# Kernel optimization log

Measured on AMD Instinct MI355X. Metric: run time of the kernel, lower is better.

## Reference

```python
import jax, jax.numpy as jnp
import numpy as np

N_NODES = 100000
N_EDGES = 3200000
D = 32


def _gat(x, edge_index, W, att_s, att_d, bias, heads, ch, neg_slope):
    """PyG-style GATConv (shared lin for src/dst, add_self_loops=False).
    x: [N, D_in], edge_index: [2, E], W: [heads*ch, D_in],
    att_s/att_d: [heads, ch], bias: [heads*ch]. Returns [N, heads*ch]."""
    n = x.shape[0]
    h = (x @ W.T).reshape(n, heads, ch)                      # [N,H,C]
    a_s = (h * att_s[None]).sum(-1)                           # [N,H]
    a_d = (h * att_d[None]).sum(-1)                           # [N,H]
    src, dst = edge_index[0], edge_index[1]
    logits = jax.nn.leaky_relu(a_s[src] + a_d[dst], neg_slope)  # [E,H]
    # segment softmax over edges grouped by destination node
    m = jax.ops.segment_max(logits, dst, num_segments=n)     # [N,H]
    m = jnp.where(jnp.isfinite(m), m, 0.0)                    # nodes w/ no in-edges
    ex = jnp.exp(logits - m[dst])                             # [E,H]
    denom = jax.ops.segment_sum(ex, dst, num_segments=n)     # [N,H]
    alpha = ex / (denom[dst] + 1e-16)                         # [E,H]
    out = jax.ops.segment_sum(alpha[:, :, None] * h[src], dst, num_segments=n)  # [N,H,C]
    return out.reshape(n, heads * ch) + bias


def setup_inputs() -> dict:
    key = jax.random.key(0)
    ks = jax.random.split(key, 16)
    x = jax.random.normal(ks[0], (N_NODES, D), dtype=jnp.float32)
    edge_index = jax.random.randint(ks[1], (2, N_EDGES), 0, N_NODES, dtype=jnp.int64)
    s = 1.0 / np.sqrt(D)
    return {
        "x": x,
        "edge_index": edge_index,
        "W1": jax.random.normal(ks[2], (32, D), dtype=jnp.float32) * s,
        "att_s1": jax.random.normal(ks[3], (2, 16), dtype=jnp.float32) * 0.05,
        "att_d1": jax.random.normal(ks[4], (2, 16), dtype=jnp.float32) * 0.05,
        "b1": jnp.full((32,), 0.1, dtype=jnp.float32),
        "ea1": jnp.ones((1,), dtype=jnp.float32),  # edge_activator
        "W2": jax.random.normal(ks[5], (32, 32), dtype=jnp.float32) * s,
        "att_s2": jax.random.normal(ks[6], (2, 16), dtype=jnp.float32) * 0.05,
        "att_d2": jax.random.normal(ks[7], (2, 16), dtype=jnp.float32) * 0.05,
        "b2": jnp.full((32,), 0.1, dtype=jnp.float32),
        "W3": jax.random.normal(ks[8], (32, 32), dtype=jnp.float32) * s,
        "att_s3": jax.random.normal(ks[9], (1, 32), dtype=jnp.float32) * 0.05,
        "att_d3": jax.random.normal(ks[10], (1, 32), dtype=jnp.float32) * 0.05,
        "b3": jnp.full((32,), 0.1, dtype=jnp.float32),
    }


def reference(x, edge_index, W1, att_s1, att_d1, b1, ea1,
              W2, att_s2, att_d2, b2, W3, att_s3, att_d3, b3):
    # --- layer 1 (negative_slope=0.01) ---
    h = _gat(x, edge_index, W1, att_s1, att_d1, b1, heads=2, ch=16, neg_slope=0.01)
    scale = jnp.tanh(ea1)[0]
    scale = jnp.where(scale < 0.1, 1.0, scale)  # 'continue' branch skips the scaling
    h = h * scale
    h = h + 0.05 * jax.lax.stop_gradient(h)      # h + 0.05*h.detach()
    h = jax.nn.elu(h)                            # eval path (training=False)
    h = jnp.clip(h, -3.0, 3.0)
    # --- layer 2 (default negative_slope=0.2) ---
    h = _gat(h, edge_index, W2, att_s2, att_d2, b2, heads=2, ch=16, neg_slope=0.2)
    h = jax.nn.elu(h)
    h = jnp.clip(h, -3.0, 3.0)
    # --- layer 3: heads=1, concat=False ---
    out = _gat(h, edge_index, W3, att_s3, att_d3, b3, heads=1, ch=32, neg_slope=0.2)
    return out
```

## Files before the change

kernel.cpp:

```cpp
#include <hip/hip_runtime.h>
#include <hip/hip_bf16.h>
#include <hip/hip_fp16.h>


#define NPB  128
#define CAPB 6144
#define PAD_SENTINEL 0xFFFFFFFFu

__global__ void __launch_bounds__(1024)
k_bin(const int* __restrict__ src, const int* __restrict__ dst,
      int* __restrict__ bucket_cursor, unsigned int* __restrict__ pairs,
      int e, int nb) {
    __shared__ int h[1024];
    __shared__ int bs[1024];
    __shared__ int cb[1024];
    __shared__ unsigned int stage[8192];
    int t = threadIdx.x;
    h[t] = 0;
    __syncthreads();
    int e4 = e >> 2;
    int base4 = blockIdx.x * 2048;
    int boff[8];
    unsigned int pk[8];
#pragma unroll
    for (int k = 0; k < 2; k++) {
        int i4 = base4 + k * 1024 + t;
        if (i4 < e4) {
            int4 dv = ((const int4*)dst)[i4];
            int4 sv = ((const int4*)src)[i4];
            const int* dd = (const int*)&dv;
            const int* ss = (const int*)&sv;
#pragma unroll
            for (int j = 0; j < 4; j++) {
                int q = 4 * k + j;
                int d = dd[j];
                int b = d >> 7;
                pk[q] = ((unsigned int)ss[j] << 7) | (unsigned int)(d & 127);
                int off = atomicAdd(&h[b], 1);
                boff[q] = (b << 16) | off;
            }
        } else {
#pragma unroll
            for (int j = 0; j < 4; j++) boff[4 * k + j] = -1;
        }
    }
    __syncthreads();
    if (t >= 128 && t - 128 < nb) {
        int b = t - 128;
        int c = h[b];
        cb[b] = c ? atomicAdd(&bucket_cursor[b], c) : 0;
    }
    if (t < 64) {
        int sum = 0;
#pragma unroll
        for (int j = 0; j < 16; j++) sum += h[t * 16 + j];
        int run = sum;
#pragma unroll
        for (int off = 1; off < 64; off <<= 1) {
            int v = __shfl_up(run, off, 64);
            if (t >= off) run += v;
        }
        int base = run - sum;
#pragma unroll
        for (int j = 0; j < 16; j++) {
            int b = t * 16 + j;
            bs[b] = base;
            base += h[b];
        }
    }
    __syncthreads();
#pragma unroll
    for (int q = 0; q < 8; q++) {
        if (boff[q] >= 0) {
            int b = boff[q] >> 16;
            stage[bs[b] + (boff[q] & 0xFFFF)] = pk[q];
        }
    }
    __syncthreads();
    int wv = t >> 6, ln = t & 63;
    for (int b = wv; b < nb; b += 16) {
        int c = h[b];
        if (c == 0) continue;
        int gb = cb[b];
        int room = CAPB - gb;
        if (c > room) c = (room > 0) ? room : 0;
        unsigned int* dp = pairs + (size_t)b * CAPB + gb;
        const unsigned int* sp = stage + bs[b];
        for (int o = ln; o < c; o += 64) dp[o] = sp[o];
    }
    if (blockIdx.x == 0 && t < (e & 3)) {
        int i = (e & ~3) + t;
        int d = dst[i];
        int b = d >> 7;
        int r = atomicAdd(&bucket_cursor[b], 1);
        if (r < CAPB)
            pairs[(size_t)b * CAPB + r] =
                ((unsigned int)src[i] << 7) | (unsigned int)(d & 127);
    }
}

__global__ void __launch_bounds__(512)
k_bucket_sort(const unsigned int* __restrict__ pairs,
              const int* __restrict__ bucket_cursor,
              int2* __restrict__ rowinfo, int* __restrict__ src_sorted,
              int n) {
    __shared__ int cnt[NPB];
    __shared__ int cur[NPB];
    __shared__ int total;
    __shared__ unsigned int lp[CAPB];
    __shared__ int op[CAPB];
    int b = blockIdx.x;
    int t = threadIdx.x;
    int bbase = b * CAPB;
    int m = bucket_cursor[b];
    if (m > CAPB) m = CAPB;
    if (t < NPB) cnt[t] = 0;
    __syncthreads();
    for (int cb = 0; cb < m; cb += 4096) {
        unsigned int pv[8];
#pragma unroll
        for (int u = 0; u < 8; u++) {
            int i = cb + u * 512 + t;
            pv[u] = (i < m) ? pairs[bbase + i] : PAD_SENTINEL;
        }
#pragma unroll
        for (int u = 0; u < 8; u++) {
            int i = cb + u * 512 + t;
            if (i < m) lp[i] = pv[u];
            if (pv[u] != PAD_SENTINEL) atomicAdd(&cnt[pv[u] & 127], 1);
        }
    }
    __syncthreads();
    if (t < 64) {
        int c0 = cnt[2 * t];
        int c1 = cnt[2 * t + 1];
        int sum = c0 + c1;
        int run = sum;
#pragma unroll
        for (int off = 1; off < 64; off <<= 1) {
            int v = __shfl_up(run, off, 64);
            if (t >= off) run += v;
        }
        int ex = run - sum;
        cur[2 * t] = ex;
        cur[2 * t + 1] = ex + c0;
        int node = b * NPB + 2 * t;
        if (node < n) rowinfo[node] = make_int2(bbase + ex, c0);
        if (node + 1 < n) rowinfo[node + 1] = make_int2(bbase + ex + c0, c1);
        if (t == 63) total = run;
    }
    __syncthreads();
    for (int cb = 0; cb < m; cb += 4096) {
        unsigned int pv[8];
        int of[8];
#pragma unroll
        for (int u = 0; u < 8; u++) {
            int i = cb + u * 512 + t;
            pv[u] = (i < m) ? lp[i] : PAD_SENTINEL;
        }
#pragma unroll
        for (int u = 0; u < 8; u++)
            if (pv[u] != PAD_SENTINEL) of[u] = atomicAdd(&cur[pv[u] & 127], 1);
#pragma unroll
        for (int u = 0; u < 8; u++)
            if (pv[u] != PAD_SENTINEL) op[of[u]] = (int)(pv[u] >> 7);
    }
    __syncthreads();
    int nt4 = (total + 3) >> 2;
    int4* dst4 = (int4*)(src_sorted + bbase);
    const int4* src4 = (const int4*)op;
    for (int i = t; i < nt4; i += 512) dst4[i] = src4[i];
}

template <int H>
__global__ void k_transform(const float* __restrict__ in, const float* __restrict__ W,
                            const float* __restrict__ att_s, const float* __restrict__ att_d,
                            __half* __restrict__ h16, float* __restrict__ a_s,
                            float* __restrict__ a_d, int n) {
    constexpr int C = 32 / H;
    __shared__ float Wl[32][33];
    __shared__ float xs[8][32];
    int t = threadIdx.x;
    for (int i = t; i < 1024; i += 256) Wl[i >> 5][i & 31] = W[i];
    int nl = t >> 5, o = t & 31;
    int node = blockIdx.x * 8 + nl;
    xs[nl][o] = (node < n) ? in[node * 32 + o] : 0.f;
    __syncthreads();
    float acc = 0.f;
#pragma unroll
    for (int k = 0; k < 32; k++) acc = fmaf(xs[nl][k], Wl[o][k], acc);
    if (node < n) {
        h16[node * 32 + o] = __float2half_rn(acc);
        float vs = acc * att_s[o];
        float vd = acc * att_d[o];
#pragma unroll
        for (int m = C / 2; m >= 1; m >>= 1) {
            vs += __shfl_xor(vs, m, 64);
            vd += __shfl_xor(vd, m, 64);
        }
        if ((o % C) == 0) {
            int hh = o / C;
            a_s[node * H + hh] = vs;
            a_d[node * H + hh] = vd;
        }
    }
}

template <int H, int EPI>
__global__ void k_edge(const int2* __restrict__ rowinfo, const int* __restrict__ src_sorted,
                       const __half* __restrict__ h16,
                       const float* __restrict__ a_s, const float* __restrict__ a_d,
                       const float* __restrict__ bias, const float* __restrict__ ea,
                       float* __restrict__ out, int n, float slope) {
    constexpr int CAP = 128;
    constexpr int RSTR = 2 * CAP + 16;
    __shared__ int lds_raw[8][H][RSTR];
    int nw = threadIdx.x >> 5;
    int hl = threadIdx.x & 31;
    int node = blockIdx.x * 8 + nw;
    if (node >= n) return;
    int2 bi = rowinfo[node];
    int beg = bi.x, deg = bi.y;
    int padB = (deg + 31) & ~31;

    float ad[H];
#pragma unroll
    for (int hh = 0; hh < H; hh++) ad[hh] = a_d[node * H + hh];

    float ds[H];
#pragma unroll
    for (int hh = 0; hh < H; hh++) ds[hh] = 0.f;
    bool fast = (padB <= CAP);
    if (fast) {
        for (int idx = hl; idx < padB; idx += 32) {
            if (idx < deg) {
                int s = src_sorted[beg + idx];
                if (H == 2) {
                    float2 as2 = *(const float2*)((const char*)a_s + (unsigned)(s << 3));
                    float l0 = as2.x + ad[0]; l0 = fmaxf(l0, l0 * slope);
                    float l1 = as2.y + ad[1]; l1 = fmaxf(l1, l1 * slope);
                    float e0 = __expf(l0), e1 = __expf(l1);
                    ds[0] += e0; ds[1] += e1;
                    ((int2*)lds_raw[nw][0])[idx] = make_int2(s, __float_as_int(e0));
                    ((int2*)lds_raw[nw][H - 1])[idx] = make_int2(s, __float_as_int(e1));
                } else {
                    float l0 = a_s[s] + ad[0]; l0 = fmaxf(l0, l0 * slope);
                    float e0 = __expf(l0);
                    ds[0] += e0;
                    ((int2*)lds_raw[nw][0])[idx] = make_int2(s, __float_as_int(e0));
                }
            } else {
#pragma unroll
                for (int hh = 0; hh < H; hh++)
                    ((int2*)lds_raw[nw][hh])[idx] = make_int2(0, 0);
            }
        }
    } else {
        for (int idx = hl; idx < deg; idx += 32) {
            int s = src_sorted[beg + idx];
            if (H == 2) {
                float2 as2 = *(const float2*)((const char*)a_s + (unsigned)(s << 3));
                float l0 = as2.x + ad[0]; l0 = fmaxf(l0, l0 * slope);
                float l1 = as2.y + ad[1]; l1 = fmaxf(l1, l1 * slope);
                ds[0] += __expf(l0); ds[1] += __expf(l1);
            } else {
                float l0 = a_s[s] + ad[0]; l0 = fmaxf(l0, l0 * slope);
                ds[0] += __expf(l0);
            }
        }
    }

    int e2 = hl >> 4;
    int l16 = hl & 15;
    int hd = (H == 2) ? (l16 >> 3) : 0;
    int co = l16 << 2;
    float adh = ad[hd];
    float acc0 = 0.f, acc1 = 0.f;
    const char* hbase = (const char*)h16;
    const int* lb = &lds_raw[nw][hd][e2 * 4];

    if (fast) {
        for (int base = 0; base < padB; base += 32) {
            int4 q[8];
#pragma unroll
            for (int u = 0; u < 8; u++)
                q[u] = *(const int4*)(lb + base * 2 + u * 8);
            __half2 hv[16];
#pragma unroll
            for (int u = 0; u < 8; u++) {
                hv[2 * u]     = *(const __half2*)(hbase + (unsigned)((q[u].x << 6) + co));
                hv[2 * u + 1] = *(const __half2*)(hbase + (unsigned)((q[u].z << 6) + co));
            }
#pragma unroll
            for (int u = 0; u < 8; u++) {
                float x0 = __int_as_float(q[u].y);
                float x1 = __int_as_float(q[u].w);
                acc0 = fmaf(x0, __half2float(__low2half(hv[2 * u])), acc0);
                acc1 = fmaf(x0, __half2float(__high2half(hv[2 * u])), acc1);
                acc0 = fmaf(x1, __half2float(__low2half(hv[2 * u + 1])), acc0);
                acc1 = fmaf(x1, __half2float(__high2half(hv[2 * u + 1])), acc1);
            }
        }
    } else {
        for (int base = 0; base < deg; base += 16) {
#pragma unroll
            for (int u = 0; u < 8; u++) {
                int idx = base + u * 2 + e2;
                int s = 0;
                float ex = 0.f;
                if (idx < deg) {
                    s = src_sorted[beg + idx];
                    float l = a_s[s * H + hd] + adh;
                    l = fmaxf(l, l * slope);
                    ex = __expf(l);
                }
                __half2 hv = *(const __half2*)(hbase + (unsigned)((s << 6) + co));
                acc0 = fmaf(ex, __half2float(__low2half(hv)), acc0);
                acc1 = fmaf(ex, __half2float(__high2half(hv)), acc1);
            }
        }
    }

#pragma unroll
    for (int hh = 0; hh < H; hh++) {
        float v = ds[hh];
#pragma unroll
        for (int m = 16; m >= 1; m >>= 1) v += __shfl_xor(v, m, 64);
        ds[hh] = 1.f / (v + 1e-16f);
    }

    acc0 += __shfl_xor(acc0, 16, 64);
    acc1 += __shfl_xor(acc1, 16, 64);

    if (l16 == hl) {
        float invd = ds[hd];
        float2 bv = *(const float2*)(bias + l16 * 2);
        float v0 = fmaf(acc0, invd, bv.x);
        float v1 = fmaf(acc1, invd, bv.y);
        if (EPI == 1) {
            float s0 = tanhf(ea[0]);
            if (s0 < 0.1f) s0 = 1.0f;
            s0 *= 1.05f;
            v0 *= s0; v1 *= s0;
            v0 = (v0 > 0.f) ? v0 : expm1f(v0);
            v1 = (v1 > 0.f) ? v1 : expm1f(v1);
            v0 = fminf(3.f, fmaxf(-3.f, v0));
            v1 = fminf(3.f, fmaxf(-3.f, v1));
        } else if (EPI == 2) {
            v0 = (v0 > 0.f) ? v0 : expm1f(v0);
            v1 = (v1 > 0.f) ? v1 : expm1f(v1);
            v0 = fminf(3.f, fmaxf(-3.f, v0));
            v1 = fminf(3.f, fmaxf(-3.f, v1));
        }
        *(float2*)(out + (size_t)node * 32 + l16 * 2) = make_float2(v0, v1);
    }
}

extern "C" void kernel_launch(void* const* d_in, const int* in_sizes, int n_in,
                              void* d_out, int out_size, void* d_ws, size_t ws_size,
                              hipStream_t stream) {
    const float* x   = (const float*)d_in[0];
    const int*   ei  = (const int*)d_in[1];
    const float* W1  = (const float*)d_in[2];
    const float* as1 = (const float*)d_in[3];
    const float* ad1 = (const float*)d_in[4];
    const float* b1  = (const float*)d_in[5];
    const float* ea1 = (const float*)d_in[6];
    const float* W2  = (const float*)d_in[7];
    const float* as2 = (const float*)d_in[8];
    const float* ad2 = (const float*)d_in[9];
    const float* b2  = (const float*)d_in[10];
    const float* W3  = (const float*)d_in[11];
    const float* as3 = (const float*)d_in[12];
    const float* ad3 = (const float*)d_in[13];
    const float* b3  = (const float*)d_in[14];
    float* out = (float*)d_out;

    const int n = in_sizes[0] / 32;
    const int e = in_sizes[1] / 2;
    const int* src = ei;
    const int* dst = ei + e;
    const int nb = (n + NPB - 1) / NPB;

    char* w = (char*)d_ws;
    auto alloc = [&](size_t bytes) -> void* {
        void* p = (void*)w;
        w += (bytes + 255) & ~(size_t)255;
        return p;
    };
    __half* h16     = (__half*)alloc((size_t)n * 32 * 2);
    float* a_s      = (float*)alloc((size_t)n * 2 * 4);
    float* a_d      = (float*)alloc((size_t)n * 2 * 4);
    float* bufA     = (float*)alloc((size_t)n * 32 * 4);
    float* bufB     = (float*)alloc((size_t)n * 32 * 4);
    int2* rowinfo   = (int2*)alloc((size_t)n * 8);
    int* bucket_cur = (int*)alloc((size_t)(nb + 1) * 4);
    int* src_sorted = (int*)alloc((size_t)nb * CAPB * 4);
    unsigned int* pairs = (unsigned int*)bufA;

    hipMemsetAsync(bucket_cur, 0, (size_t)nb * 4, stream);
    int e4 = e >> 2;
    k_bin<<<(e4 + 2047) / 2048, 1024, 0, stream>>>(src, dst, bucket_cur, pairs, e, nb);
    k_bucket_sort<<<nb, 512, 0, stream>>>(pairs, bucket_cur, rowinfo, src_sorted, n);

    const int tgrid = (n + 7) / 8;
    const int egrid = (n + 7) / 8;

    k_transform<2><<<tgrid, 256, 0, stream>>>(x, W1, as1, ad1, h16, a_s, a_d, n);
    k_edge<2, 1><<<egrid, 256, 0, stream>>>(rowinfo, src_sorted, h16, a_s, a_d, b1, ea1, bufA, n, 0.01f);

    k_transform<2><<<tgrid, 256, 0, stream>>>(bufA, W2, as2, ad2, h16, a_s, a_d, n);
    k_edge<2, 2><<<egrid, 256, 0, stream>>>(rowinfo, src_sorted, h16, a_s, a_d, b2, nullptr, bufB, n, 0.2f);

    k_transform<1><<<tgrid, 256, 0, stream>>>(bufB, W3, as3, ad3, h16, a_s, a_d, n);
    k_edge<1, 0><<<egrid, 256, 0, stream>>>(rowinfo, src_sorted, h16, a_s, a_d, b3, nullptr, out, n, 0.2f);
}
```

Baseline: 346.1 us.

## Split fp16 features into per-half planes and process each half in separate blocks

The transformed fp16 features are stored as two planes of 16 channels each, and a_s/a_d become head-major. The edge-kernel grid is doubled so each block aggregates one channel half (or one head) for 8 nodes. This halves the gather working set per pass so it is more likely to stay in L2, and each warp now covers 4 edges per step with 8 lanes per row. In exchange, the edge indices are read and the logits and exps are computed twice per edge. Nontemporal loads for src_sorted and nontemporal output stores are also added.

```diff
diff --git a/kernel.cpp b/kernel.cpp
--- a/kernel.cpp
+++ b/kernel.cpp
@@ -175,8 +175,8 @@
 template <int H>
 __global__ void k_transform(const float* __restrict__ in, const float* __restrict__ W,
                             const float* __restrict__ att_s, const float* __restrict__ att_d,
-                            __half* __restrict__ h16, float* __restrict__ a_s,
-                            float* __restrict__ a_d, int n) {
+                            __half* __restrict__ h16a, __half* __restrict__ h16b,
+                            float* __restrict__ a_s, float* __restrict__ a_d, int n) {
     constexpr int C = 32 / H;
     __shared__ float Wl[32][33];
     __shared__ float xs[8][32];
@@ -190,7 +190,8 @@
 #pragma unroll
     for (int k = 0; k < 32; k++) acc = fmaf(xs[nl][k], Wl[o][k], acc);
     if (node < n) {
-        h16[node * 32 + o] = __float2half_rn(acc);
+        __half* hp = (o < 16) ? h16a : h16b;
+        hp[node * 16 + (o & 15)] = __float2half_rn(acc);
         float vs = acc * att_s[o];
         float vd = acc * att_d[o];
 #pragma unroll
@@ -200,121 +201,99 @@
         }
         if ((o % C) == 0) {
             int hh = o / C;
-            a_s[node * H + hh] = vs;
-            a_d[node * H + hh] = vd;
+            a_s[hh * n + node] = vs;
+            a_d[hh * n + node] = vd;
         }
     }
 }
 
 template <int H, int EPI>
 __global__ void k_edge(const int2* __restrict__ rowinfo, const int* __restrict__ src_sorted,
-                       const __half* __restrict__ h16,
+                       const __half* __restrict__ h16a, const __half* __restrict__ h16b,
                        const float* __restrict__ a_s, const float* __restrict__ a_d,
                        const float* __restrict__ bias, const float* __restrict__ ea,
                        float* __restrict__ out, int n, float slope) {
     constexpr int CAP = 128;
     constexpr int RSTR = 2 * CAP + 16;
-    __shared__ int lds_raw[8][H][RSTR];
+    __shared__ int lds_raw[8][RSTR];
+    int head = blockIdx.x & 1;
+    int grp = blockIdx.x >> 1;
     int nw = threadIdx.x >> 5;
     int hl = threadIdx.x & 31;
-    int node = blockIdx.x * 8 + nw;
+    int node = grp * 8 + nw;
     if (node >= n) return;
     int2 bi = rowinfo[node];
     int beg = bi.x, deg = bi.y;
-    int padB = (deg + 31) & ~31;
-
-    float ad[H];
-#pragma unroll
-    for (int hh = 0; hh < H; hh++) ad[hh] = a_d[node * H + hh];
-
-    float ds[H];
-#pragma unroll
-    for (int hh = 0; hh < H; hh++) ds[hh] = 0.f;
+    int padB = (deg + 15) & ~15;
+
+    const __half* hsrc = head ? h16b : h16a;
+    const float* asp = a_s + (H == 2 ? head * n : 0);
+    float adv = a_d[(H == 2 ? head * n : 0) + node];
+
+    float dsum = 0.f;
     bool fast = (padB <= CAP);
     if (fast) {
         for (int idx = hl; idx < padB; idx += 32) {
             if (idx < deg) {
-                int s = src_sorted[beg + idx];
-                if (H == 2) {
-                    float2 as2 = *(const float2*)((const char*)a_s + (unsigned)(s << 3));
-                    float l0 = as2.x + ad[0]; l0 = fmaxf(l0, l0 * slope);
-                    float l1 = as2.y + ad[1]; l1 = fmaxf(l1, l1 * slope);
-                    float e0 = __expf(l0), e1 = __expf(l1);
-                    ds[0] += e0; ds[1] += e1;
-                    ((int2*)lds_raw[nw][0])[idx] = make_int2(s, __float_as_int(e0));
-                    ((int2*)lds_raw[nw][H - 1])[idx] = make_int2(s, __float_as_int(e1));
-                } else {
-                    float l0 = a_s[s] + ad[0]; l0 = fmaxf(l0, l0 * slope);
-                    float e0 = __expf(l0);
-                    ds[0] += e0;
-                    ((int2*)lds_raw[nw][0])[idx] = make_int2(s, __float_as_int(e0));
-                }
+                int s = __builtin_nontemporal_load(src_sorted + beg + idx);
+                float l = asp[s] + adv;
+                l = fmaxf(l, l * slope);
+                float e0 = __expf(l);
+                dsum += e0;
+                ((int2*)lds_raw[nw])[idx] = make_int2(s, __float_as_int(e0));
             } else {
-#pragma unroll
-                for (int hh = 0; hh < H; hh++)
-                    ((int2*)lds_raw[nw][hh])[idx] = make_int2(0, 0);
+                ((int2*)lds_raw[nw])[idx] = make_int2(0, 0);
             }
         }
     } else {
         for (int idx = hl; idx < deg; idx += 32) {
-            int s = src_sorted[beg + idx];
-            if (H == 2) {
-                float2 as2 = *(const float2*)((const char*)a_s + (unsigned)(s << 3));
-                float l0 = as2.x + ad[0]; l0 = fmaxf(l0, l0 * slope);
-                float l1 = as2.y + ad[1]; l1 = fmaxf(l1, l1 * slope);
-                ds[0] += __expf(l0); ds[1] += __expf(l1);
-            } else {
-                float l0 = a_s[s] + ad[0]; l0 = fmaxf(l0, l0 * slope);
-                ds[0] += __expf(l0);
-            }
-        }
-    }
-
-    int e2 = hl >> 4;
-    int l16 = hl & 15;
-    int hd = (H == 2) ? (l16 >> 3) : 0;
-    int co = l16 << 2;
-    float adh = ad[hd];
+            int s = __builtin_nontemporal_load(src_sorted + beg + idx);
+            float l = asp[s] + adv;
+            l = fmaxf(l, l * slope);
+            dsum += __expf(l);
+        }
+    }
+
+    int e4 = hl >> 3;
+    int l8 = hl & 7;
+    int co = l8 << 2;
     float acc0 = 0.f, acc1 = 0.f;
-    const char* hbase = (const char*)h16;
-    const int* lb = &lds_raw[nw][hd][e2 * 4];
+    const char* hbase = (const char*)hsrc;
 
     if (fast) {
-        for (int base = 0; base < padB; base += 32) {
-            int4 q[8];
-#pragma unroll
-            for (int u = 0; u < 8; u++)
-                q[u] = *(const int4*)(lb + base * 2 + u * 8);
-            __half2 hv[16];
-#pragma unroll
-            for (int u = 0; u < 8; u++) {
-                hv[2 * u]     = *(const __half2*)(hbase + (unsigned)((q[u].x << 6) + co));
-                hv[2 * u + 1] = *(const __half2*)(hbase + (unsigned)((q[u].z << 6) + co));
-            }
-#pragma unroll
-            for (int u = 0; u < 8; u++) {
-                float x0 = __int_as_float(q[u].y);
-                float x1 = __int_as_float(q[u].w);
-                acc0 = fmaf(x0, __half2float(__low2half(hv[2 * u])), acc0);
-                acc1 = fmaf(x0, __half2float(__high2half(hv[2 * u])), acc1);
-                acc0 = fmaf(x1, __half2float(__low2half(hv[2 * u + 1])), acc0);
-                acc1 = fmaf(x1, __half2float(__high2half(hv[2 * u + 1])), acc1);
-            }
+        const int* lb = lds_raw[nw] + 4 * e4;
+        for (int base = 0; base < padB; base += 16) {
+            int4 q0 = *(const int4*)(lb + 2 * base);
+            int4 q1 = *(const int4*)(lb + 2 * base + 16);
+            __half2 h0 = *(const __half2*)(hbase + (unsigned)((q0.x << 5) + co));
+            __half2 h1 = *(const __half2*)(hbase + (unsigned)((q0.z << 5) + co));
+            __half2 h2 = *(const __half2*)(hbase + (unsigned)((q1.x << 5) + co));
+            __half2 h3 = *(const __half2*)(hbase + (unsigned)((q1.z << 5) + co));
+            float x0 = __int_as_float(q0.y), x1 = __int_as_float(q0.w);
+            float x2 = __int_as_float(q1.y), x3 = __int_as_float(q1.w);
+            acc0 = fmaf(x0, __half2float(__low2half(h0)), acc0);
+            acc1 = fmaf(x0, __half2float(__high2half(h0)), acc1);
+            acc0 = fmaf(x1, __half2float(__low2half(h1)), acc0);
+            acc1 = fmaf(x1, __half2float(__high2half(h1)), acc1);
+            acc0 = fmaf(x2, __half2float(__low2half(h2)), acc0);
+            acc1 = fmaf(x2, __half2float(__high2half(h2)), acc1);
+            acc0 = fmaf(x3, __half2float(__low2half(h3)), acc0);
+            acc1 = fmaf(x3, __half2float(__high2half(h3)), acc1);
         }
     } else {
         for (int base = 0; base < deg; base += 16) {
 #pragma unroll
-            for (int u = 0; u < 8; u++) {
-                int idx = base + u * 2 + e2;
+            for (int j = 0; j < 4; j++) {
+                int idx = base + e4 * 4 + j;
                 int s = 0;
                 float ex = 0.f;
                 if (idx < deg) {
-                    s = src_sorted[beg + idx];
-                    float l = a_s[s * H + hd] + adh;
+                    s = __builtin_nontemporal_load(src_sorted + beg + idx);
+                    float l = asp[s] + adv;
                     l = fmaxf(l, l * slope);
                     ex = __expf(l);
                 }
-                __half2 hv = *(const __half2*)(hbase + (unsigned)((s << 6) + co));
+                __half2 hv = *(const __half2*)(hbase + (unsigned)((s << 5) + co));
                 acc0 = fmaf(ex, __half2float(__low2half(hv)), acc0);
                 acc1 = fmaf(ex, __half2float(__high2half(hv)), acc1);
             }
@@ -322,19 +301,17 @@
     }
 
 #pragma unroll
-    for (int hh = 0; hh < H; hh++) {
-        float v = ds[hh];
-#pragma unroll
-        for (int m = 16; m >= 1; m >>= 1) v += __shfl_xor(v, m, 64);
-        ds[hh] = 1.f / (v + 1e-16f);
-    }
-
+    for (int m = 16; m >= 1; m >>= 1) dsum += __shfl_xor(dsum, m, 64);
+    float invd = 1.f / (dsum + 1e-16f);
+
+    acc0 += __shfl_xor(acc0, 8, 64);
+    acc1 += __shfl_xor(acc1, 8, 64);
     acc0 += __shfl_xor(acc0, 16, 64);
     acc1 += __shfl_xor(acc1, 16, 64);
 
-    if (l16 == hl) {
-        float invd = ds[hd];
-        float2 bv = *(const float2*)(bias + l16 * 2);
+    if (hl < 8) {
+        int ch = (head << 4) + l8 * 2;
+        float2 bv = *(const float2*)(bias + ch);
         float v0 = fmaf(acc0, invd, bv.x);
         float v1 = fmaf(acc1, invd, bv.y);
         if (EPI == 1) {
@@ -352,7 +329,9 @@
             v0 = fminf(3.f, fmaxf(-3.f, v0));
             v1 = fminf(3.f, fmaxf(-3.f, v1));
         }
-        *(float2*)(out + (size_t)node * 32 + l16 * 2) = make_float2(v0, v1);
+        float2 r = make_float2(v0, v1);
+        __builtin_nontemporal_store(*reinterpret_cast<const double*>(&r),
+                                    reinterpret_cast<double*>(out + (size_t)node * 32 + ch));
     }
 }
 
@@ -388,7 +367,8 @@
         w += (bytes + 255) & ~(size_t)255;
         return p;
     };
-    __half* h16     = (__half*)alloc((size_t)n * 32 * 2);
+    __half* h16a    = (__half*)alloc((size_t)n * 16 * 2);
+    __half* h16b    = (__half*)alloc((size_t)n * 16 * 2);
     float* a_s      = (float*)alloc((size_t)n * 2 * 4);
     float* a_d      = (float*)alloc((size_t)n * 2 * 4);
     float* bufA     = (float*)alloc((size_t)n * 32 * 4);
@@ -404,14 +384,14 @@
     k_bucket_sort<<<nb, 512, 0, stream>>>(pairs, bucket_cur, rowinfo, src_sorted, n);
 
     const int tgrid = (n + 7) / 8;
-    const int egrid = (n + 7) / 8;
-
-    k_transform<2><<<tgrid, 256, 0, stream>>>(x, W1, as1, ad1, h16, a_s, a_d, n);
-    k_edge<2, 1><<<egrid, 256, 0, stream>>>(rowinfo, src_sorted, h16, a_s, a_d, b1, ea1, bufA, n, 0.01f);
-
-    k_transform<2><<<tgrid, 256, 0, stream>>>(bufA, W2, as2, ad2, h16, a_s, a_d, n);
-    k_edge<2, 2><<<egrid, 256, 0, stream>>>(rowinfo, src_sorted, h16, a_s, a_d, b2, nullptr, bufB, n, 0.2f);
-
-    k_transform<1><<<tgrid, 256, 0, stream>>>(bufB, W3, as3, ad3, h16, a_s, a_d, n);
-    k_edge<1, 0><<<egrid, 256, 0, stream>>>(rowinfo, src_sorted, h16, a_s, a_d, b3, nullptr, out, n, 0.2f);
-}
+    const int egrid = 2 * ((n + 7) / 8);
+
+    k_transform<2><<<tgrid, 256, 0, stream>>>(x, W1, as1, ad1, h16a, h16b, a_s, a_d, n);
+    k_edge<2, 1><<<egrid, 256, 0, stream>>>(rowinfo, src_sorted, h16a, h16b, a_s, a_d, b1, ea1, bufA, n, 0.01f);
+
+    k_transform<2><<<tgrid, 256, 0, stream>>>(bufA, W2, as2, ad2, h16a, h16b, a_s, a_d, n);
+    k_edge<2, 2><<<egrid, 256, 0, stream>>>(rowinfo, src_sorted, h16a, h16b, a_s, a_d, b2, nullptr, bufB, n, 0.2f);
+
+    k_transform<1><<<tgrid, 256, 0, stream>>>(bufB, W3, as3, ad3, h16a, h16b, a_s, a_d, n);
+    k_edge<1, 0><<<egrid, 256, 0, stream>>>(rowinfo, src_sorted, h16a, h16b, a_s, a_d, b3, nullptr, out, n, 0.2f);
+}
```

Result: slower. 432.3 us (+24.9%).
